# Kernel optimization log

Hardware: AMD Instinct MI355X
Metric: run time of the kernel (lower is better)

## Reference

```python
import jax, jax.numpy as jnp
import numpy as np

BS = 128      # outer batch (was bs=8 in original)
NR = 3        # num_ref
C_DATA = 64
C_GT = 3
C_HID = 256
H = W = 32


def setup_inputs() -> dict:
    key = jax.random.key(0)
    k1, k2, k3, k4 = jax.random.split(key, 4)
    data = jax.random.normal(k1, (BS * NR, C_DATA, H, W), dtype=jnp.float32)
    gt = jax.random.normal(k2, (BS, C_GT, H, W), dtype=jnp.float32)
    # 1x1 conv weights == per-pixel dense layers
    W1 = jax.random.normal(k3, (C_HID, C_DATA + C_GT), dtype=jnp.float32) * 0.05
    b1 = jnp.zeros((C_HID,), dtype=jnp.float32)
    W3 = jax.random.normal(k4, (1, C_HID), dtype=jnp.float32) * 0.05
    b3 = jnp.zeros((1,), dtype=jnp.float32)
    return {"data": data, "gt": gt, "W1": W1, "b1": b1, "W3": W3, "b3": b3}


def reference(data, gt, W1, b1, W3, b3):
    # data: [BS*NR, 64, H, W] -> [BS, NR, 64, H, W]
    d = data.reshape(BS, NR, C_DATA, H, W)
    # gt[i] repeated over NR refs -> broadcast instead of looping over batch
    g = jnp.broadcast_to(gt[:, None], (BS, NR, C_GT, H, W))
    x = jnp.concatenate([d, g], axis=2)                      # [BS, NR, 67, H, W]
    # 1x1 conv -> relu  (feature_1)
    f1 = jax.nn.relu(jnp.einsum('bnchw,oc->bnohw', x, W1)
                     + b1[None, None, :, None, None])        # [BS, NR, 256, H, W]
    # 1x1 conv -> sigmoid (feature_3, feature_4)
    s = jax.nn.sigmoid(jnp.einsum('bnchw,oc->bnohw', f1, W3)
                       + b3[None, None, :, None, None])      # [BS, NR, 1, H, W]
    # normalize weights over the num_ref dim (torch dim=0 within each batch item)
    w = s / jnp.sum(s, axis=1, keepdims=True)                # [BS, NR, 1, H, W]
    # weighted sum over refs; w broadcasts over the 64 channels
    z = jnp.sum(d * w, axis=1)                               # [BS, 64, H, W]
    return z, w
```

## Files before the change

kernel.cpp:

```cpp
#include <hip/hip_runtime.h>
#include <hip/hip_bf16.h>

#define BS 128
#define NR 3
#define CD 64
#define CG 3
#define CH 256
#define HW 1024
#define K_IN 67
#define P 64

typedef __attribute__((ext_vector_type(4))) short bf16x4;
typedef __attribute__((ext_vector_type(8))) short bf16x8;
typedef __attribute__((ext_vector_type(4))) float f32x4;

static __device__ __forceinline__ short f2bf(float x) {
    union { __hip_bfloat16 b; short s; } c;
    c.b = __float2bfloat16(x);
    return c.s;
}
static __device__ __forceinline__ float bf2f(short s) {
    union { unsigned u; float f; } c;
    c.u = (unsigned)(unsigned short)s << 16;
    return c.f;
}

__global__ __launch_bounds__(256) void prep_kernel(
    const float* __restrict__ W1, const float* __restrict__ b1,
    short* __restrict__ w1f)
{
    const int fid  = blockIdx.x * 256 + threadIdx.x;
    const int mt   = fid / 192;
    const int rem  = fid % 192;
    const int t    = rem >> 6;
    const int lane = rem & 63;
    const int row  = mt * 16 + (lane & 15);
    const int k0   = t * 32 + (lane >> 4) * 8;
    bf16x8 v;
#pragma unroll
    for (int j = 0; j < 8; ++j) {
        const int k = k0 + j;
        float val = 0.f;
        if (k < K_IN)       val = W1[row * K_IN + k];
        else if (k == K_IN) val = b1[row];
        v[j] = f2bf(val);
    }
    *(bf16x8*)&w1f[(size_t)fid * 8] = v;
}

__global__ __launch_bounds__(256, 4) void fused_kernel(
    const float* __restrict__ data, const float* __restrict__ gt,
    const short* __restrict__ w1f, const float* __restrict__ W3,
    const float* __restrict__ b3, float* __restrict__ out)
{
    __shared__ short xls[NR * 16 * P * 4];
    __shared__ short gtp[P * 4];
    __shared__ short zp[P * 4];
    __shared__ float p_lds[4][NR * P];
    __shared__ float s_lds[NR][P];
    __shared__ float w_lds[NR][P];

    const int tid  = threadIdx.x;
    const int lane = tid & 63;
    const int wave = tid >> 6;
    const int b    = blockIdx.x >> 4;
    const int pt0  = (blockIdx.x & 15) * P;
    const int col  = lane & 15, kq = lane >> 4;

    bf16x8 afrag[4][3];
#pragma unroll
    for (int i = 0; i < 4; ++i)
#pragma unroll
        for (int t = 0; t < 3; ++t)
            afrag[i][t] = *(const bf16x8*)&w1f[(((size_t)(wave * 4 + i) * 3 + t) * 64 + lane) * 8];
    float w3v[4][4];
#pragma unroll
    for (int i = 0; i < 4; ++i)
#pragma unroll
        for (int r = 0; r < 4; ++r)
            w3v[i][r] = W3[wave * 64 + i * 16 + kq * 4 + r];

    if (tid < P) *(bf16x4*)&zp[tid * 4] = (bf16x4){0, 0, 0, 0};
    {
        const int c = tid >> 6, px = tid & 63;
        if (c < CG) gtp[px * 4 + c] = f2bf(gt[((size_t)b * CG + c) * HW + pt0 + px]);
        else        gtp[px * 4 + 3] = (short)0x3F80;
    }

#pragma unroll
    for (int half = 0; half < 2; ++half) {
        float4 ld[6];
#pragma unroll
        for (int u = 0; u < 6; ++u) {
            const int q = (half * 6 + u) * 256 + tid;
            const int ref = q >> 10, ch = (q >> 4) & 63, p4 = q & 15;
            ld[u] = *(const float4*)(data + ((size_t)(b * NR + ref) * CD + ch) * HW + pt0 + 4 * p4);
        }
#pragma unroll
        for (int u = 0; u < 6; ++u) {
            const int q = (half * 6 + u) * 256 + tid;
            const int ref = q >> 10, ch = (q >> 4) & 63, p4 = q & 15;
            short* xp = &xls[((ref * 16 + (ch >> 2)) * P + 4 * p4) * 4 + (ch & 3)];
            xp[0]  = f2bf(ld[u].x);
            xp[4]  = f2bf(ld[u].y);
            xp[8]  = f2bf(ld[u].z);
            xp[12] = f2bf(ld[u].w);
        }
    }

    __syncthreads();

#pragma unroll
    for (int nt = 0; nt < NR * 4; ++nt) {
        const int ref = nt >> 2, pn0 = (nt & 3) * 16;
        bf16x8 bfrag[3];
#pragma unroll
        for (int t = 0; t < 3; ++t) {
            const short* plo;
            const short* phi;
            if (t < 2) {
                const int c2 = t * 8 + kq * 2;
                plo = &xls[((ref * 16 + c2)     * P) * 4];
                phi = &xls[((ref * 16 + c2 + 1) * P) * 4];
            } else {
                plo = (kq == 0) ? gtp : zp;
                phi = zp;
            }
            const bf16x4 lo = *(const bf16x4*)&plo[(pn0 + col) * 4];
            const bf16x4 hi = *(const bf16x4*)&phi[(pn0 + col) * 4];
            bfrag[t] = __builtin_shufflevector(lo, hi, 0, 1, 2, 3, 4, 5, 6, 7);
        }

        f32x4 acc[4];
#pragma unroll
        for (int i = 0; i < 4; ++i) acc[i] = (f32x4){0.f, 0.f, 0.f, 0.f};
#pragma unroll
        for (int t = 0; t < 3; ++t)
#pragma unroll
            for (int i = 0; i < 4; ++i)
                acc[i] = __builtin_amdgcn_mfma_f32_16x16x32_bf16(
                    afrag[i][t], bfrag[t], acc[i], 0, 0, 0);

        float partial = 0.f;
#pragma unroll
        for (int i = 0; i < 4; ++i)
#pragma unroll
            for (int r = 0; r < 4; ++r)
                partial += w3v[i][r] * fmaxf(acc[i][r], 0.f);
        partial += __shfl_xor(partial, 16);
        partial += __shfl_xor(partial, 32);
        if (lane < 16) p_lds[wave][ref * P + pn0 + lane] = partial;
    }
    __syncthreads();

    if (tid < NR * P) {
        const float t = p_lds[0][tid] + p_lds[1][tid] + p_lds[2][tid]
                      + p_lds[3][tid] + b3[0];
        s_lds[tid >> 6][tid & 63] = 1.f / (1.f + __expf(-t));
    }
    __syncthreads();

    float* wout = out + (size_t)BS * CD * HW;
    if (tid < P) {
        const float s0 = s_lds[0][tid], s1 = s_lds[1][tid], s2 = s_lds[2][tid];
        const float inv = 1.f / (s0 + s1 + s2);
        const float w0 = s0 * inv, w1 = s1 * inv, w2 = s2 * inv;
        w_lds[0][tid] = w0; w_lds[1][tid] = w1; w_lds[2][tid] = w2;
        wout[((size_t)b * NR + 0) * HW + pt0 + tid] = w0;
        wout[((size_t)b * NR + 1) * HW + pt0 + tid] = w1;
        wout[((size_t)b * NR + 2) * HW + pt0 + tid] = w2;
    }
    __syncthreads();

#pragma unroll
    for (int u = 0; u < 4; ++u) {
        const int q = u * 256 + tid;
        const int ch = q >> 4, p4 = q & 15;
        float zx = 0.f, zy = 0.f, zz = 0.f, zw = 0.f;
#pragma unroll
        for (int ref = 0; ref < NR; ++ref) {
            const float4 wv = *(const float4*)&w_lds[ref][4 * p4];
            const short* xp = &xls[((ref * 16 + (ch >> 2)) * P + 4 * p4) * 4 + (ch & 3)];
            zx += wv.x * bf2f(xp[0]);
            zy += wv.y * bf2f(xp[4]);
            zz += wv.z * bf2f(xp[8]);
            zw += wv.w * bf2f(xp[12]);
        }
        const float4 zv = {zx, zy, zz, zw};
        *(float4*)(out + ((size_t)b * CD + ch) * HW + pt0 + 4 * p4) = zv;
    }
}

extern "C" void kernel_launch(void* const* d_in, const int* in_sizes, int n_in,
                              void* d_out, int out_size, void* d_ws, size_t ws_size,
                              hipStream_t stream)
{
    const float* data = (const float*)d_in[0];
    const float* gt   = (const float*)d_in[1];
    const float* W1   = (const float*)d_in[2];
    const float* b1   = (const float*)d_in[3];
    const float* W3   = (const float*)d_in[4];
    const float* b3   = (const float*)d_in[5];
    float* out  = (float*)d_out;
    short* w1f  = (short*)d_ws;

    prep_kernel<<<12, 256, 0, stream>>>(W1, b1, w1f);
    fused_kernel<<<BS * (HW / P), 256, 0, stream>>>(data, gt, w1f, W3, b3, out);
}
```

Measured before the change: 174.3 us.

## Swizzle LDS staging layout, interleave weight loads with data loads, drop w_lds sync

```diff
diff --git a/kernel.cpp b/kernel.cpp
--- a/kernel.cpp
+++ b/kernel.cpp
@@ -5,7 +5,6 @@
 #define NR 3
 #define CD 64
 #define CG 3
-#define CH 256
 #define HW 1024
 #define K_IN 67
 #define P 64
@@ -23,6 +22,10 @@
     union { unsigned u; float f; } c;
     c.u = (unsigned)(unsigned short)s << 16;
     return c.f;
+}
+
+static __device__ __forceinline__ int xoff(int ref, int c2, int px) {
+    return (((ref * 16 + c2) * 64 + px) * 8) ^ ((((c2 ^ (px >> 4)) & 3) << 5));
 }
 
 __global__ __launch_bounds__(256) void prep_kernel(
@@ -48,17 +51,16 @@
     *(bf16x8*)&w1f[(size_t)fid * 8] = v;
 }
 
-__global__ __launch_bounds__(256, 4) void fused_kernel(
+__global__ __launch_bounds__(256, 5) void fused_kernel(
     const float* __restrict__ data, const float* __restrict__ gt,
     const short* __restrict__ w1f, const float* __restrict__ W3,
     const float* __restrict__ b3, float* __restrict__ out)
 {
-    __shared__ short xls[NR * 16 * P * 4];
+    __shared__ __align__(16) char xls[NR * 16 * P * 8];
     __shared__ short gtp[P * 4];
     __shared__ short zp[P * 4];
     __shared__ float p_lds[4][NR * P];
     __shared__ float s_lds[NR][P];
-    __shared__ float w_lds[NR][P];
 
     const int tid  = threadIdx.x;
     const int lane = tid & 63;
@@ -67,19 +69,6 @@
     const int pt0  = (blockIdx.x & 15) * P;
     const int col  = lane & 15, kq = lane >> 4;
 
-    bf16x8 afrag[4][3];
-#pragma unroll
-    for (int i = 0; i < 4; ++i)
-#pragma unroll
-        for (int t = 0; t < 3; ++t)
-            afrag[i][t] = *(const bf16x8*)&w1f[(((size_t)(wave * 4 + i) * 3 + t) * 64 + lane) * 8];
-    float w3v[4][4];
-#pragma unroll
-    for (int i = 0; i < 4; ++i)
-#pragma unroll
-        for (int r = 0; r < 4; ++r)
-            w3v[i][r] = W3[wave * 64 + i * 16 + kq * 4 + r];
-
     if (tid < P) *(bf16x4*)&zp[tid * 4] = (bf16x4){0, 0, 0, 0};
     {
         const int c = tid >> 6, px = tid & 63;
@@ -87,24 +76,41 @@
         else        gtp[px * 4 + 3] = (short)0x3F80;
     }
 
-#pragma unroll
-    for (int half = 0; half < 2; ++half) {
-        float4 ld[6];
-#pragma unroll
-        for (int u = 0; u < 6; ++u) {
-            const int q = (half * 6 + u) * 256 + tid;
-            const int ref = q >> 10, ch = (q >> 4) & 63, p4 = q & 15;
-            ld[u] = *(const float4*)(data + ((size_t)(b * NR + ref) * CD + ch) * HW + pt0 + 4 * p4);
-        }
-#pragma unroll
-        for (int u = 0; u < 6; ++u) {
-            const int q = (half * 6 + u) * 256 + tid;
-            const int ref = q >> 10, ch = (q >> 4) & 63, p4 = q & 15;
-            short* xp = &xls[((ref * 16 + (ch >> 2)) * P + 4 * p4) * 4 + (ch & 3)];
-            xp[0]  = f2bf(ld[u].x);
-            xp[4]  = f2bf(ld[u].y);
-            xp[8]  = f2bf(ld[u].z);
-            xp[12] = f2bf(ld[u].w);
+    bf16x8 afrag[4][3];
+    float  w3v[4][4];
+#pragma unroll
+    for (int pass = 0; pass < 3; ++pass) {
+        float ld[4][4];
+#pragma unroll
+        for (int u = 0; u < 4; ++u) {
+            const int uid = (pass * 4 + u) * 256 + tid;
+            const int ref = uid >> 10, c2 = (uid >> 6) & 15, px = uid & 63;
+            const float* dp = data + ((size_t)(b * NR + ref) * CD + 4 * c2) * HW + pt0 + px;
+#pragma unroll
+            for (int i = 0; i < 4; ++i) ld[u][i] = dp[(size_t)i * HW];
+        }
+        if (pass == 0) {
+#pragma unroll
+            for (int i = 0; i < 4; ++i)
+#pragma unroll
+                for (int t = 0; t < 3; ++t)
+                    afrag[i][t] = *(const bf16x8*)&w1f[(((size_t)(wave * 4 + i) * 3 + t) * 64 + lane) * 8];
+        }
+        if (pass == 1) {
+#pragma unroll
+            for (int i = 0; i < 4; ++i)
+#pragma unroll
+                for (int r = 0; r < 4; ++r)
+                    w3v[i][r] = W3[wave * 64 + i * 16 + kq * 4 + r];
+        }
+#pragma unroll
+        for (int u = 0; u < 4; ++u) {
+            const int uid = (pass * 4 + u) * 256 + tid;
+            const int ref = uid >> 10, c2 = (uid >> 6) & 15, px = uid & 63;
+            bf16x4 v;
+#pragma unroll
+            for (int i = 0; i < 4; ++i) v[i] = f2bf(ld[u][i]);
+            *(bf16x4*)&xls[xoff(ref, c2, px)] = v;
         }
     }
 
@@ -113,33 +119,33 @@
 #pragma unroll
     for (int nt = 0; nt < NR * 4; ++nt) {
         const int ref = nt >> 2, pn0 = (nt & 3) * 16;
+        const int px  = pn0 + col;
         bf16x8 bfrag[3];
 #pragma unroll
-        for (int t = 0; t < 3; ++t) {
-            const short* plo;
-            const short* phi;
-            if (t < 2) {
-                const int c2 = t * 8 + kq * 2;
-                plo = &xls[((ref * 16 + c2)     * P) * 4];
-                phi = &xls[((ref * 16 + c2 + 1) * P) * 4];
-            } else {
-                plo = (kq == 0) ? gtp : zp;
-                phi = zp;
-            }
-            const bf16x4 lo = *(const bf16x4*)&plo[(pn0 + col) * 4];
-            const bf16x4 hi = *(const bf16x4*)&phi[(pn0 + col) * 4];
+        for (int t = 0; t < 2; ++t) {
+            const int c2 = t * 8 + kq * 2;
+            const bf16x4 lo = *(const bf16x4*)&xls[xoff(ref, c2, px)];
+            const bf16x4 hi = *(const bf16x4*)&xls[xoff(ref, c2 + 1, px)];
             bfrag[t] = __builtin_shufflevector(lo, hi, 0, 1, 2, 3, 4, 5, 6, 7);
         }
+        {
+            const bf16x4 lo = (kq == 0) ? *(const bf16x4*)&gtp[px * 4]
+                                        : *(const bf16x4*)&zp[px * 4];
+            const bf16x4 hi = *(const bf16x4*)&zp[px * 4];
+            bfrag[2] = __builtin_shufflevector(lo, hi, 0, 1, 2, 3, 4, 5, 6, 7);
+        }
 
         f32x4 acc[4];
 #pragma unroll
         for (int i = 0; i < 4; ++i) acc[i] = (f32x4){0.f, 0.f, 0.f, 0.f};
+        __builtin_amdgcn_s_setprio(1);
 #pragma unroll
         for (int t = 0; t < 3; ++t)
 #pragma unroll
             for (int i = 0; i < 4; ++i)
                 acc[i] = __builtin_amdgcn_mfma_f32_16x16x32_bf16(
                     afrag[i][t], bfrag[t], acc[i], 0, 0, 0);
+        __builtin_amdgcn_s_setprio(0);
 
         float partial = 0.f;
 #pragma unroll
@@ -161,33 +167,31 @@
     __syncthreads();
 
     float* wout = out + (size_t)BS * CD * HW;
-    if (tid < P) {
-        const float s0 = s_lds[0][tid], s1 = s_lds[1][tid], s2 = s_lds[2][tid];
+#pragma unroll
+    for (int v = 0; v < 4; ++v) {
+        const int vid = v * 256 + tid;
+        const int c2 = vid >> 6, px = vid & 63;
+        const float s0 = s_lds[0][px], s1 = s_lds[1][px], s2 = s_lds[2][px];
         const float inv = 1.f / (s0 + s1 + s2);
-        const float w0 = s0 * inv, w1 = s1 * inv, w2 = s2 * inv;
-        w_lds[0][tid] = w0; w_lds[1][tid] = w1; w_lds[2][tid] = w2;
-        wout[((size_t)b * NR + 0) * HW + pt0 + tid] = w0;
-        wout[((size_t)b * NR + 1) * HW + pt0 + tid] = w1;
-        wout[((size_t)b * NR + 2) * HW + pt0 + tid] = w2;
-    }
-    __syncthreads();
-
-#pragma unroll
-    for (int u = 0; u < 4; ++u) {
-        const int q = u * 256 + tid;
-        const int ch = q >> 4, p4 = q & 15;
-        float zx = 0.f, zy = 0.f, zz = 0.f, zw = 0.f;
+        if (v == 0 && c2 < NR) {
+            const float sv = (c2 == 0) ? s0 : (c2 == 1) ? s1 : s2;
+            wout[((size_t)b * NR + c2) * HW + pt0 + px] = sv * inv;
+        }
+        float z0 = 0.f, z1 = 0.f, z2 = 0.f, z3 = 0.f;
 #pragma unroll
         for (int ref = 0; ref < NR; ++ref) {
-            const float4 wv = *(const float4*)&w_lds[ref][4 * p4];
-            const short* xp = &xls[((ref * 16 + (ch >> 2)) * P + 4 * p4) * 4 + (ch & 3)];
-            zx += wv.x * bf2f(xp[0]);
-            zy += wv.y * bf2f(xp[4]);
-            zz += wv.z * bf2f(xp[8]);
-            zw += wv.w * bf2f(xp[12]);
-        }
-        const float4 zv = {zx, zy, zz, zw};
-        *(float4*)(out + ((size_t)b * CD + ch) * HW + pt0 + 4 * p4) = zv;
+            const float w = ((ref == 0) ? s0 : (ref == 1) ? s1 : s2) * inv;
+            const bf16x4 d = *(const bf16x4*)&xls[xoff(ref, c2, px)];
+            z0 += w * bf2f(d[0]);
+            z1 += w * bf2f(d[1]);
+            z2 += w * bf2f(d[2]);
+            z3 += w * bf2f(d[3]);
+        }
+        float* zout = out + ((size_t)b * CD + 4 * c2) * HW + pt0 + px;
+        zout[0 * HW] = z0;
+        zout[1 * HW] = z1;
+        zout[2 * HW] = z2;
+        zout[3 * HW] = z3;
     }
 }
 
```

Result: slower. 333.3 us (+91.2%).
